# Kernel tuning notes

Hardware: AMD Instinct MI355X
Metric: run time of the kernel (lower is better)

## Reference

```python
import jax, jax.numpy as jnp
import numpy as np

N = 50000      # rows of A == cols of A (square constraint/variable graph)
NNZ = 1_600_000
D = 128        # x_size == y_size == out_size (forced by the module's wiring)


def spmm(rows, cols, vals, X, n_out):
    # out[r] = sum_{e: rows[e]==r} vals[e] * X[cols[e]]
    return jax.ops.segment_sum(vals[:, None] * X[cols], rows, num_segments=n_out)


def _linear(z, w, b):
    return z @ w.T + b


def setup_inputs() -> dict:
    key = jax.random.key(0)
    ks = jax.random.split(key, 20)
    f = lambda i, shape, s=1.0: jax.random.normal(ks[i], shape, dtype=jnp.float32) * s
    w_scale = 1.0 / np.sqrt(D)
    return {
        "x": f(0, (N, D)),
        "y": f(1, (N, D)),
        "c": f(2, (N, 1)),
        "b": f(3, (N, 1)),
        "A_vals": f(4, (NNZ,)),
        "A_rows": jax.random.randint(ks[5], (NNZ,), 0, N),
        "A_cols": jax.random.randint(ks[6], (NNZ,), 0, N),
        "Ukx_w": f(7, (D, D), w_scale), "Ukx_b": f(8, (D,), w_scale),
        "Uky_w": f(9, (D, D), w_scale), "Uky_b": f(10, (D,), w_scale),
        "tau": f(11, (1,)),
        "Vky_w": f(12, (D, D), w_scale), "Vky_b": f(13, (D,), w_scale),
        "Wkx_w": f(14, (D, D), w_scale), "Wkx_b": f(15, (D,), w_scale),
        "Vkx_w": f(16, (D, D), w_scale), "Vkx_b": f(17, (D,), w_scale),
        "sigma": f(18, (1,)),
    }


def reference(x, y, c, b, A_vals, A_rows, A_cols,
              Ukx_w, Ukx_b, Uky_w, Uky_b, tau,
              Vky_w, Vky_b, Wkx_w, Wkx_b, Vkx_w, Vkx_b, sigma):
    # --- pdhg_layer_x: x <- relu(Ukx(x) - tau * (c @ ones(1,D) - AT @ Uky(y))) ---
    # c @ ones(1, D) is just broadcasting c:[N,1] to [N,D].
    uy = _linear(y, Uky_w, Uky_b)                      # [N, D]
    at_uy = spmm(A_cols, A_rows, A_vals, uy, N)        # AT spmm: swap row/col indices
    x_new = jax.nn.relu(_linear(x, Ukx_w, Ukx_b) - tau * (c - at_uy))

    # --- pdhg_layer_y: y <- relu(Vky(y) - sigma * (b@ones - 2*A@Wkx(x') + A@Vkx(x'))) ---
    wx = _linear(x_new, Wkx_w, Wkx_b)                  # [N, D]
    vx = _linear(x_new, Vkx_w, Vkx_b)                  # [N, D]
    a_wx = spmm(A_rows, A_cols, A_vals, wx, N)
    a_vx = spmm(A_rows, A_cols, A_vals, vx, N)
    y_new = jax.nn.relu(_linear(y, Vky_w, Vky_b) - sigma * (b - 2.0 * a_wx + a_vx))
    return (x_new, y_new)
```

## Files before the change

### kernel.cpp

```cpp
#include <hip/hip_runtime.h>

#define D 128
#define RB 64
#define NBKMAX 1024
#define CH 256

__device__ __forceinline__ unsigned short bf16r(float f) {
    unsigned b = __float_as_uint(f);
    return (unsigned short)((b + 0x7FFFu + ((b >> 16) & 1u)) >> 16);
}

__global__ __launch_bounds__(256) void setup_weights(
    const float* __restrict__ Uky, const float* __restrict__ Ukx,
    const float* __restrict__ Vky, const float* __restrict__ Vkx,
    const float* __restrict__ Wkx, const float* __restrict__ Vkx_b,
    const float* __restrict__ Wkx_b,
    float* __restrict__ UkyT, float* __restrict__ UkxT,
    float* __restrict__ VkyT, float* __restrict__ WcT, float* __restrict__ bc)
{
    const int m = blockIdx.x;
    const float* src = (m == 0) ? Uky : (m == 1) ? Ukx : (m == 2) ? Vky : nullptr;
    float* dst = (m == 0) ? UkyT : (m == 1) ? UkxT : (m == 2) ? VkyT : WcT;
    for (int i = threadIdx.x; i < D * D; i += 256) {
        int k = i >> 7, d = i & 127;
        float v;
        if (m == 3) v = Vkx[d * D + k] - 2.0f * Wkx[d * D + k];
        else        v = src[d * D + k];
        dst[i] = v;
    }
    if (m == 3 && threadIdx.x < D)
        bc[threadIdx.x] = Vkx_b[threadIdx.x] - 2.0f * Wkx_b[threadIdx.x];
}

template <int EPI, int OB16>
__global__ __launch_bounds__(256) void gemm_v2(
    const float* __restrict__ X, const float* __restrict__ WT,
    const float* __restrict__ bias, const float* __restrict__ colvec,
    const float* __restrict__ spout, const float* __restrict__ scal,
    float* __restrict__ out, int N)
{
    __shared__ float Xs[64][D + 4];
    __shared__ float Wt[64][D + 4];
    const int t = threadIdx.x;
    const int block_row = blockIdx.x * 64;

#pragma unroll
    for (int i = 0; i < 8; ++i) {
        int f = t + i * 256;
        int r = f >> 5;
        int k4 = (f & 31) << 2;
        float4 g = make_float4(0.f, 0.f, 0.f, 0.f);
        int row = block_row + r;
        if (row < N) g = *reinterpret_cast<const float4*>(&X[(size_t)row * D + k4]);
        *reinterpret_cast<float4*>(&Xs[r][k4]) = g;
    }

    const int cg = t & 15;
    const int rp = t >> 4;
    const int r0 = rp * 4;
    const int c0 = cg * 4, c1 = 64 + cg * 4;

    float acc[4][8] = {{0.f}};

    for (int kb = 0; kb < D; kb += 64) {
        __syncthreads();
#pragma unroll
        for (int i = 0; i < 8; ++i) {
            int f = t + i * 256;
            int kk = f >> 5;
            int d4 = (f & 31) << 2;
            float4 g = *reinterpret_cast<const float4*>(&WT[(size_t)(kb + kk) * D + d4]);
            *reinterpret_cast<float4*>(&Wt[kk][d4]) = g;
        }
        __syncthreads();
#pragma unroll 2
        for (int k4 = 0; k4 < 64; k4 += 4) {
            float4 xr[4];
#pragma unroll
            for (int j = 0; j < 4; ++j)
                xr[j] = *reinterpret_cast<const float4*>(&Xs[r0 + j][kb + k4]);
#pragma unroll
            for (int q = 0; q < 4; ++q) {
                const float4 w0 = *reinterpret_cast<const float4*>(&Wt[k4 + q][c0]);
                const float4 w1 = *reinterpret_cast<const float4*>(&Wt[k4 + q][c1]);
#pragma unroll
                for (int j = 0; j < 4; ++j) {
                    const float xv = (q == 0) ? xr[j].x : (q == 1) ? xr[j].y
                                   : (q == 2) ? xr[j].z : xr[j].w;
                    acc[j][0] += xv * w0.x; acc[j][1] += xv * w0.y;
                    acc[j][2] += xv * w0.z; acc[j][3] += xv * w0.w;
                    acc[j][4] += xv * w1.x; acc[j][5] += xv * w1.y;
                    acc[j][6] += xv * w1.z; acc[j][7] += xv * w1.w;
                }
            }
        }
    }

    const float sc = (EPI == 0) ? 0.f : scal[0];
    const float4 bias0 = *reinterpret_cast<const float4*>(&bias[c0]);
    const float4 bias1 = *reinterpret_cast<const float4*>(&bias[c1]);

#pragma unroll
    for (int j = 0; j < 4; ++j) {
        const int row = block_row + r0 + j;
        if (row >= N) continue;
        const float cv = (EPI == 0) ? 0.f : colvec[row];
#pragma unroll
        for (int h = 0; h < 2; ++h) {
            const int col = (h == 0) ? c0 : c1;
            const float4 bs = (h == 0) ? bias0 : bias1;
            float4 res;
            res.x = acc[j][h * 4 + 0] + bs.x;
            res.y = acc[j][h * 4 + 1] + bs.y;
            res.z = acc[j][h * 4 + 2] + bs.z;
            res.w = acc[j][h * 4 + 3] + bs.w;
            if (EPI == 1) {
                float4 sp = *reinterpret_cast<const float4*>(&spout[(size_t)row * D + col]);
                res.x = fmaxf(res.x - sc * (cv - sp.x), 0.f);
                res.y = fmaxf(res.y - sc * (cv - sp.y), 0.f);
                res.z = fmaxf(res.z - sc * (cv - sp.z), 0.f);
                res.w = fmaxf(res.w - sc * (cv - sp.w), 0.f);
            } else if (EPI == 2) {
                float4 sp = *reinterpret_cast<const float4*>(&spout[(size_t)row * D + col]);
                res.x = fmaxf(res.x - sc * (cv + sp.x), 0.f);
                res.y = fmaxf(res.y - sc * (cv + sp.y), 0.f);
                res.z = fmaxf(res.z - sc * (cv + sp.z), 0.f);
                res.w = fmaxf(res.w - sc * (cv + sp.w), 0.f);
            }
            if (OB16) {
                unsigned short* ob = (unsigned short*)out;
                ushort4 r16;
                r16.x = bf16r(res.x); r16.y = bf16r(res.y);
                r16.z = bf16r(res.z); r16.w = bf16r(res.w);
                *reinterpret_cast<ushort4*>(&ob[(size_t)row * D + col]) = r16;
            } else {
                *reinterpret_cast<float4*>(&out[(size_t)row * D + col]) = res;
            }
        }
    }
}

__global__ __launch_bounds__(256) void hist_chunks(
    const int* __restrict__ rows, const int* __restrict__ cols,
    int* __restrict__ hR, int* __restrict__ hC, int nnz, int nbk, int ce)
{
    __shared__ int lh[NBKMAX];
    const int chunk = blockIdx.x;
    const bool isC = blockIdx.y;
    const int* idx = isC ? cols : rows;
    int* hout = (isC ? hC : hR) + (size_t)chunk * nbk;
    for (int i = threadIdx.x; i < nbk; i += 256) lh[i] = 0;
    __syncthreads();
    const int e0 = chunk * ce, e1 = min(nnz, e0 + ce);
    for (int e = e0 + threadIdx.x; e < e1; e += 256)
        atomicAdd(&lh[idx[e] >> 6], 1);
    __syncthreads();
    for (int i = threadIdx.x; i < nbk; i += 256) hout[i] = lh[i];
}

__global__ __launch_bounds__(256) void bucket_tot(
    const int* __restrict__ hR, const int* __restrict__ hC,
    int* __restrict__ cntR, int* __restrict__ cntC, int nbk)
{
    const int b = blockIdx.x;
    const bool isC = blockIdx.y;
    const int* h = (isC ? hC : hR);
    __shared__ int s[256];
    int v = h[(size_t)threadIdx.x * nbk + b];
    s[threadIdx.x] = v;
    __syncthreads();
#pragma unroll
    for (int d = 128; d > 0; d >>= 1) {
        if (threadIdx.x < d) s[threadIdx.x] += s[threadIdx.x + d];
        __syncthreads();
    }
    if (threadIdx.x == 0) (isC ? cntC : cntR)[b] = s[0];
}

__global__ __launch_bounds__(256) void scan_buckets(
    const int* __restrict__ cntR, const int* __restrict__ cntC,
    int* __restrict__ goffR, int* __restrict__ goffC, int nbk)
{
    const int* cnt = blockIdx.x ? cntC : cntR;
    int* goff = blockIdx.x ? goffC : goffR;
    __shared__ int s[256];
    const int t = threadIdx.x;
    const int base = t * 4;
    int loc[4]; int sum = 0;
#pragma unroll
    for (int u = 0; u < 4; ++u) {
        int idx = base + u;
        int v = (idx < nbk) ? cnt[idx] : 0;
        loc[u] = sum; sum += v;
    }
    s[t] = sum;
    __syncthreads();
#pragma unroll
    for (int d = 1; d < 256; d <<= 1) {
        int tv = (t >= d) ? s[t - d] : 0;
        __syncthreads();
        s[t] += tv;
        __syncthreads();
    }
    int excl = s[t] - sum;
#pragma unroll
    for (int u = 0; u < 4; ++u) {
        int idx = base + u;
        if (idx < nbk) goff[idx] = excl + loc[u];
    }
}

__global__ __launch_bounds__(256) void runstarts(
    int* __restrict__ hR, int* __restrict__ hC,
    const int* __restrict__ goffR, const int* __restrict__ goffC, int nbk)
{
    const int b = blockIdx.x;
    const bool isC = blockIdx.y;
    int* h = (isC ? hC : hR);
    const int g0 = (isC ? goffC : goffR)[b];
    __shared__ int s[256];
    const int t = threadIdx.x;
    int v = h[(size_t)t * nbk + b];
    s[t] = v;
    __syncthreads();
#pragma unroll
    for (int d = 1; d < 256; d <<= 1) {
        int tv = (t >= d) ? s[t - d] : 0;
        __syncthreads();
        s[t] += tv;
        __syncthreads();
    }
    h[(size_t)t * nbk + b] = g0 + s[t] - v;
}

__global__ __launch_bounds__(256) void scatter_chunks(
    const int* __restrict__ rows, const int* __restrict__ cols,
    const float* __restrict__ vals,
    const int* __restrict__ rsR, int2* __restrict__ recR,
    const int* __restrict__ rsC, int2* __restrict__ recC,
    int nnz, int nbk, int ce)
{
    __shared__ int lrsR[NBKMAX], lcurR[NBKMAX];
    __shared__ int lrsC[NBKMAX], lcurC[NBKMAX];
    const int chunk = blockIdx.x;
    for (int i = threadIdx.x; i < nbk; i += 256) {
        lrsR[i] = rsR[(size_t)chunk * nbk + i]; lcurR[i] = 0;
        lrsC[i] = rsC[(size_t)chunk * nbk + i]; lcurC[i] = 0;
    }
    __syncthreads();
    const int e0 = chunk * ce, e1 = min(nnz, e0 + ce);
    for (int e = e0 + threadIdx.x; e < e1; e += 256) {
        int r = rows[e], c = cols[e];
        int vb = __float_as_int(vals[e]);
        int bR = r >> 6, bC = c >> 6;
        int pR = lrsR[bR] + atomicAdd(&lcurR[bR], 1);
        recR[pR] = make_int2(((r & 63) << 16) | c, vb);
        int pC = lrsC[bC] + atomicAdd(&lcurC[bC], 1);
        recC[pC] = make_int2(((c & 63) << 16) | r, vb);
    }
}

__global__ __launch_bounds__(256) void sort_buckets(
    const int2* __restrict__ recR, const int2* __restrict__ recC,
    const int* __restrict__ goffR, const int* __restrict__ cntR,
    const int* __restrict__ goffC, const int* __restrict__ cntC,
    unsigned* __restrict__ pairsR, unsigned* __restrict__ pairsC,
    int* __restrict__ offR, int* __restrict__ lenR,
    int* __restrict__ offC, int* __restrict__ lenC, int N)
{
    const bool isC = blockIdx.y;
    const int b = blockIdx.x;
    const int2* rec = isC ? recC : recR;
    unsigned* pairs = isC ? pairsC : pairsR;
    int* off = isC ? offC : offR;
    int* len = isC ? lenC : lenR;
    const int s = (isC ? goffC : goffR)[b];
    const int L = (isC ? cntC : cntR)[b];
    const int t = threadIdx.x;

    __shared__ int lcnt[RB], lpos[RB], lcur[RB];
    if (t < RB) lcnt[t] = 0;
    __syncthreads();
    for (int i = t; i < L; i += 256)
        atomicAdd(&lcnt[rec[s + i].x >> 16], 1);
    __syncthreads();
    if (t == 0) {
        int run = 0;
#pragma unroll
        for (int r = 0; r < RB; ++r) { lpos[r] = run; run += lcnt[r]; }
    }
    __syncthreads();
    if (t < RB) {
        int row = b * RB + t;
        if (row < N) { off[row] = s + lpos[t]; len[row] = lcnt[t]; }
        lcur[t] = 0;
    }
    __syncthreads();
    for (int i = t; i < L; i += 256) {
        int2 pr = rec[s + i];
        int r = pr.x >> 16;
        int p = lpos[r] + atomicAdd(&lcur[r], 1);
        unsigned vb = (unsigned)pr.y;
        unsigned v16 = (vb + 0x7FFFu + ((vb >> 16) & 1u)) >> 16;
        pairs[s + p] = (v16 << 16) | (unsigned)(pr.x & 0xFFFF);
    }
}

__global__ __launch_bounds__(256) void spmm_pairs_v3(
    const unsigned* __restrict__ pairs, const int* __restrict__ off,
    const int* __restrict__ len, const unsigned short* __restrict__ Xb,
    float* __restrict__ out, int N)
{
    const int row = (blockIdx.x * 256 + threadIdx.x) >> 6;
    if (row >= N) return;
    const int lane = threadIdx.x & 63;
    const int half = lane >> 5;
    const int cq = (lane & 31) << 2;
    const int s = off[row];
    const int L = len[row];

    float4 a0 = make_float4(0.f, 0.f, 0.f, 0.f);
    float4 a1 = make_float4(0.f, 0.f, 0.f, 0.f);
    float4 a2 = make_float4(0.f, 0.f, 0.f, 0.f);
    float4 a3 = make_float4(0.f, 0.f, 0.f, 0.f);

#define BF(u) __uint_as_float((unsigned)(u) << 16)
    int i = 0;
    for (; i + 7 < L; i += 8) {
        unsigned p0 = pairs[s + i + 0 + half];
        unsigned p1 = pairs[s + i + 2 + half];
        unsigned p2 = pairs[s + i + 4 + half];
        unsigned p3 = pairs[s + i + 6 + half];
        ushort4 x0 = *reinterpret_cast<const ushort4*>(&Xb[(size_t)(p0 & 0xFFFFu) * D + cq]);
        ushort4 x1 = *reinterpret_cast<const ushort4*>(&Xb[(size_t)(p1 & 0xFFFFu) * D + cq]);
        ushort4 x2 = *reinterpret_cast<const ushort4*>(&Xb[(size_t)(p2 & 0xFFFFu) * D + cq]);
        ushort4 x3 = *reinterpret_cast<const ushort4*>(&Xb[(size_t)(p3 & 0xFFFFu) * D + cq]);
        float v0 = __uint_as_float(p0 & 0xFFFF0000u);
        float v1 = __uint_as_float(p1 & 0xFFFF0000u);
        float v2 = __uint_as_float(p2 & 0xFFFF0000u);
        float v3 = __uint_as_float(p3 & 0xFFFF0000u);
        a0.x += v0 * BF(x0.x); a0.y += v0 * BF(x0.y); a0.z += v0 * BF(x0.z); a0.w += v0 * BF(x0.w);
        a1.x += v1 * BF(x1.x); a1.y += v1 * BF(x1.y); a1.z += v1 * BF(x1.z); a1.w += v1 * BF(x1.w);
        a2.x += v2 * BF(x2.x); a2.y += v2 * BF(x2.y); a2.z += v2 * BF(x2.z); a2.w += v2 * BF(x2.w);
        a3.x += v3 * BF(x3.x); a3.y += v3 * BF(x3.y); a3.z += v3 * BF(x3.z); a3.w += v3 * BF(x3.w);
    }
    for (; i < L; i += 2) {
        int e = i + half;
        unsigned p = (e < L) ? pairs[s + e] : 0u;
        ushort4 xv = *reinterpret_cast<const ushort4*>(&Xb[(size_t)(p & 0xFFFFu) * D + cq]);
        float v = __uint_as_float(p & 0xFFFF0000u);
        a0.x += v * BF(xv.x); a0.y += v * BF(xv.y); a0.z += v * BF(xv.z); a0.w += v * BF(xv.w);
    }
#undef BF

    float4 A;
    A.x = (a0.x + a1.x) + (a2.x + a3.x);
    A.y = (a0.y + a1.y) + (a2.y + a3.y);
    A.z = (a0.z + a1.z) + (a2.z + a3.z);
    A.w = (a0.w + a1.w) + (a2.w + a3.w);
    A.x += __shfl_xor(A.x, 32);
    A.y += __shfl_xor(A.y, 32);
    A.z += __shfl_xor(A.z, 32);
    A.w += __shfl_xor(A.w, 32);
    if (half == 0)
        *reinterpret_cast<float4*>(&out[(size_t)row * D + cq]) = A;
}

__global__ __launch_bounds__(256) void spmm_atomic(
    const float* __restrict__ vals, const int* __restrict__ orow,
    const int* __restrict__ gcol, const float* __restrict__ Xm,
    float* __restrict__ outm, int nnz)
{
    const int gwave = (blockIdx.x * 256 + threadIdx.x) >> 6;
    const int lane = threadIdx.x & 63;
    const int e0 = gwave * 4;
#pragma unroll
    for (int i = 0; i < 4; ++i) {
        int e = e0 + i;
        if (e >= nnz) break;
        float v = vals[e];
        int r = orow[e];
        int c = gcol[e];
        float2 xv = *reinterpret_cast<const float2*>(&Xm[(size_t)c * D + lane * 2]);
        unsafeAtomicAdd(&outm[(size_t)r * D + lane * 2 + 0], v * xv.x);
        unsafeAtomicAdd(&outm[(size_t)r * D + lane * 2 + 1], v * xv.y);
    }
}

extern "C" void kernel_launch(void* const* d_in, const int* in_sizes, int n_in,
                              void* d_out, int out_size, void* d_ws, size_t ws_size,
                              hipStream_t stream) {
    const float* x      = (const float*)d_in[0];
    const float* y      = (const float*)d_in[1];
    const float* c      = (const float*)d_in[2];
    const float* b      = (const float*)d_in[3];
    const float* A_vals = (const float*)d_in[4];
    const int*   A_rows = (const int*)d_in[5];
    const int*   A_cols = (const int*)d_in[6];
    const float* Ukx_w  = (const float*)d_in[7];
    const float* Ukx_b  = (const float*)d_in[8];
    const float* Uky_w  = (const float*)d_in[9];
    const float* Uky_b  = (const float*)d_in[10];
    const float* tau    = (const float*)d_in[11];
    const float* Vky_w  = (const float*)d_in[12];
    const float* Vky_b  = (const float*)d_in[13];
    const float* Wkx_w  = (const float*)d_in[14];
    const float* Wkx_b  = (const float*)d_in[15];
    const float* Vkx_w  = (const float*)d_in[16];
    const float* Vkx_b  = (const float*)d_in[17];
    const float* sigma  = (const float*)d_in[18];

    const int N   = in_sizes[0] / D;
    const int nnz = in_sizes[4];
    const int nbk = (N + RB - 1) / RB;

    float* out_x = (float*)d_out;
    float* out_y = out_x + (size_t)N * D;

    const int gemm_grid = (N + 63) / 64;
    const int ggrid = (N + 3) / 4;

    const size_t pool = (size_t)nnz;
    char* base = (char*)d_ws;
    float* tmp = (float*)base;
    int2* recR = (int2*)base;
    int2* recC = recR + pool;
    size_t region0 = (size_t)N * D * 4;
    if (2 * pool * 8 > region0) region0 = 2 * pool * 8;
    char* pers = base + region0;
    float* UkyT = (float*)pers;
    float* UkxT = UkyT + D * D;
    float* VkyT = UkxT + D * D;
    float* WcT  = VkyT + D * D;
    float* bc   = WcT + D * D;
    unsigned* pairsR = (unsigned*)(bc + D);
    unsigned* pairsC = pairsR + pool;
    int* cntR  = (int*)(pairsC + pool);
    int* cntC  = cntR + nbk;
    int* goffR = cntC + nbk;
    int* goffC = goffR + nbk;
    int* offR  = goffC + nbk;
    int* lenR  = offR + N;
    int* offC  = lenR + N;
    int* lenC  = offC + N;
    int* hR = (int*)pairsR;
    int* hC = hR + (size_t)CH * nbk;

    unsigned short* uyb = (unsigned short*)out_y;
    unsigned short* zxb = (unsigned short*)tmp;

    size_t need = region0 + (4 * (size_t)D * D + D) * 4 + 2 * pool * 4
                + (4 * (size_t)nbk + 4 * (size_t)N) * 4;
    bool h_fits = (size_t)2 * CH * nbk * 4 <= pool * 4;

    setup_weights<<<4, 256, 0, stream>>>(Uky_w, Ukx_w, Vky_w, Vkx_w, Wkx_w,
                                         Vkx_b, Wkx_b, UkyT, UkxT, VkyT, WcT, bc);

    if (N < 65536 && nbk <= NBKMAX && ws_size >= need && h_fits) {
        const int ce = (nnz + CH - 1) / CH;

        {
            dim3 g1(CH, 2);
            hist_chunks<<<g1, 256, 0, stream>>>(A_rows, A_cols, hR, hC, nnz, nbk, ce);
            dim3 g2(nbk, 2);
            bucket_tot<<<g2, 256, 0, stream>>>(hR, hC, cntR, cntC, nbk);
            scan_buckets<<<2, 256, 0, stream>>>(cntR, cntC, goffR, goffC, nbk);
            runstarts<<<g2, 256, 0, stream>>>(hR, hC, goffR, goffC, nbk);
            scatter_chunks<<<CH, 256, 0, stream>>>(A_rows, A_cols, A_vals,
                                                   hR, recR, hC, recC, nnz, nbk, ce);
            sort_buckets<<<g2, 256, 0, stream>>>(recR, recC, goffR, cntR, goffC, cntC,
                                                 pairsR, pairsC, offR, lenR, offC, lenC, N);
        }

        gemm_v2<0, 1><<<gemm_grid, 256, 0, stream>>>(y, UkyT, Uky_b, nullptr, nullptr, nullptr,
                                                     (float*)uyb, N);
        spmm_pairs_v3<<<ggrid, 256, 0, stream>>>(pairsC, offC, lenC, uyb, out_x, N);
        gemm_v2<1, 0><<<gemm_grid, 256, 0, stream>>>(x, UkxT, Ukx_b, c, out_x, tau, out_x, N);
        gemm_v2<0, 1><<<gemm_grid, 256, 0, stream>>>(out_x, WcT, bc, nullptr, nullptr, nullptr,
                                                     (float*)zxb, N);
        spmm_pairs_v3<<<ggrid, 256, 0, stream>>>(pairsR, offR, lenR, zxb, out_y, N);
        gemm_v2<2, 0><<<gemm_grid, 256, 0, stream>>>(y, VkyT, Vky_b, b, out_y, sigma, out_y, N);
    } else {
        const int spmm_grid = (nnz + 15) / 16;
        gemm_v2<0, 0><<<gemm_grid, 256, 0, stream>>>(y, UkyT, Uky_b, nullptr, nullptr, nullptr, tmp, N);
        hipMemsetAsync(out_x, 0, (size_t)N * D * sizeof(float), stream);
        spmm_atomic<<<spmm_grid, 256, 0, stream>>>(A_vals, A_cols, A_rows, tmp, out_x, nnz);
        gemm_v2<1, 0><<<gemm_grid, 256, 0, stream>>>(x, UkxT, Ukx_b, c, out_x, tau, out_x, N);
        gemm_v2<0, 0><<<gemm_grid, 256, 0, stream>>>(out_x, WcT, bc, nullptr, nullptr, nullptr, tmp, N);
        hipMemsetAsync(out_y, 0, (size_t)N * D * sizeof(float), stream);
        spmm_atomic<<<spmm_grid, 256, 0, stream>>>(A_vals, A_rows, A_cols, tmp, out_y, nnz);
        gemm_v2<2, 0><<<gemm_grid, 256, 0, stream>>>(y, VkyT, Vky_b, b, out_y, sigma, out_y, N);
    }
}
```

Baseline: 330.0 us.

## Use bf16 MFMA for dense linear layers and widen scatter blocks

Replaces the fp32 SIMT GEMM in the fast path with a bf16 MFMA kernel (16x16x32). It converts the X tile to bf16 into XOR-swizzled shared memory and reads the pre-converted bf16 weights directly from global memory. Setup now also builds bf16 copies of the weights, and the fallback path keeps the fp32 GEMM. Separately, scatter_chunks moves to 1024-thread blocks. The aim is less FMA-bound GEMM time, at the cost of bf16 rounding of inputs and weights and more shared-memory atomic contention per block in scatter.

New measurement: 293.9 us. 11.0% less time.

```diff
diff --git a/kernel.cpp b/kernel.cpp
--- a/kernel.cpp
+++ b/kernel.cpp
@@ -4,6 +4,9 @@
 #define RB 64
 #define NBKMAX 1024
 #define CH 256
+
+typedef __attribute__((ext_vector_type(4))) float f32x4;
+typedef __attribute__((ext_vector_type(8))) short bf16x8;
 
 __device__ __forceinline__ unsigned short bf16r(float f) {
     unsigned b = __float_as_uint(f);
@@ -16,31 +19,45 @@
     const float* __restrict__ Wkx, const float* __restrict__ Vkx_b,
     const float* __restrict__ Wkx_b,
     float* __restrict__ UkyT, float* __restrict__ UkxT,
-    float* __restrict__ VkyT, float* __restrict__ WcT, float* __restrict__ bc)
+    float* __restrict__ VkyT, float* __restrict__ WcT,
+    unsigned short* __restrict__ UkyB, unsigned short* __restrict__ UkxB,
+    unsigned short* __restrict__ VkyB, unsigned short* __restrict__ WcB,
+    float* __restrict__ bc)
 {
     const int m = blockIdx.x;
-    const float* src = (m == 0) ? Uky : (m == 1) ? Ukx : (m == 2) ? Vky : nullptr;
-    float* dst = (m == 0) ? UkyT : (m == 1) ? UkxT : (m == 2) ? VkyT : WcT;
-    for (int i = threadIdx.x; i < D * D; i += 256) {
-        int k = i >> 7, d = i & 127;
-        float v;
-        if (m == 3) v = Vkx[d * D + k] - 2.0f * Wkx[d * D + k];
-        else        v = src[d * D + k];
-        dst[i] = v;
-    }
-    if (m == 3 && threadIdx.x < D)
-        bc[threadIdx.x] = Vkx_b[threadIdx.x] - 2.0f * Wkx_b[threadIdx.x];
+    if (m < 4) {
+        const float* src = (m == 0) ? Uky : (m == 1) ? Ukx : (m == 2) ? Vky : nullptr;
+        float* dst = (m == 0) ? UkyT : (m == 1) ? UkxT : (m == 2) ? VkyT : WcT;
+        for (int i = threadIdx.x; i < D * D; i += 256) {
+            int k = i >> 7, d = i & 127;
+            float v;
+            if (m == 3) v = Vkx[d * D + k] - 2.0f * Wkx[d * D + k];
+            else        v = src[d * D + k];
+            dst[i] = v;
+        }
+        if (m == 3 && threadIdx.x < D)
+            bc[threadIdx.x] = Vkx_b[threadIdx.x] - 2.0f * Wkx_b[threadIdx.x];
+    } else {
+        const int mm = m - 4;
+        const float* src = (mm == 0) ? Uky : (mm == 1) ? Ukx : (mm == 2) ? Vky : nullptr;
+        unsigned short* dst = (mm == 0) ? UkyB : (mm == 1) ? UkxB : (mm == 2) ? VkyB : WcB;
+        for (int i = threadIdx.x; i < D * D; i += 256) {
+            float v;
+            if (mm == 3) v = Vkx[i] - 2.0f * Wkx[i];
+            else         v = src[i];
+            dst[i] = bf16r(v);
+        }
+    }
 }
 
 template <int EPI, int OB16>
-__global__ __launch_bounds__(256) void gemm_v2(
-    const float* __restrict__ X, const float* __restrict__ WT,
+__global__ __launch_bounds__(256) void gemm_mfma(
+    const float* __restrict__ X, const unsigned short* __restrict__ Wb,
     const float* __restrict__ bias, const float* __restrict__ colvec,
     const float* __restrict__ spout, const float* __restrict__ scal,
     float* __restrict__ out, int N)
 {
-    __shared__ float Xs[64][D + 4];
-    __shared__ float Wt[64][D + 4];
+    __shared__ __align__(16) unsigned short Xs[64 * 128];
     const int t = threadIdx.x;
     const int block_row = blockIdx.x * 64;
 
@@ -52,14 +69,90 @@
         float4 g = make_float4(0.f, 0.f, 0.f, 0.f);
         int row = block_row + r;
         if (row < N) g = *reinterpret_cast<const float4*>(&X[(size_t)row * D + k4]);
-        *reinterpret_cast<float4*>(&Xs[r][k4]) = g;
+        ushort4 h;
+        h.x = bf16r(g.x); h.y = bf16r(g.y); h.z = bf16r(g.z); h.w = bf16r(g.w);
+        unsigned byte = (unsigned)(k4 * 2) ^ ((unsigned)(r & 7) << 4);
+        *reinterpret_cast<ushort4*>((char*)Xs + r * 256 + byte) = h;
+    }
+    __syncthreads();
+
+    const int w  = t >> 6;
+    const int l  = t & 63;
+    const int lr = l & 15;
+    const int lq = l >> 4;
+
+    f32x4 acc[8];
+#pragma unroll
+    for (int nt = 0; nt < 8; ++nt) acc[nt] = (f32x4)(0.f);
+
+    const int arow = w * 16 + lr;
+
+#pragma unroll
+    for (int kc = 0; kc < 4; ++kc) {
+        unsigned abyte = ((unsigned)(kc * 64 + lq * 16)) ^ ((unsigned)(arow & 7) << 4);
+        bf16x8 a = *reinterpret_cast<const bf16x8*>((const char*)Xs + arow * 256 + abyte);
+#pragma unroll
+        for (int nt = 0; nt < 8; ++nt) {
+            bf16x8 b = *reinterpret_cast<const bf16x8*>(
+                &Wb[(size_t)(nt * 16 + lr) * D + kc * 32 + lq * 8]);
+            acc[nt] = __builtin_amdgcn_mfma_f32_16x16x32_bf16(a, b, acc[nt], 0, 0, 0);
+        }
+    }
+
+    const float sc = (EPI == 0) ? 0.f : scal[0];
+    float bs[8];
+#pragma unroll
+    for (int nt = 0; nt < 8; ++nt) bs[nt] = bias[nt * 16 + lr];
+
+#pragma unroll
+    for (int r = 0; r < 4; ++r) {
+        const int row = block_row + w * 16 + lq * 4 + r;
+        if (row >= N) continue;
+        const float cv = (EPI == 0) ? 0.f : colvec[row];
+#pragma unroll
+        for (int nt = 0; nt < 8; ++nt) {
+            const int col = nt * 16 + lr;
+            float res = acc[nt][r] + bs[nt];
+            if (EPI == 1) {
+                float sp = spout[(size_t)row * D + col];
+                res = fmaxf(res - sc * (cv - sp), 0.f);
+            } else if (EPI == 2) {
+                float sp = spout[(size_t)row * D + col];
+                res = fmaxf(res - sc * (cv + sp), 0.f);
+            }
+            if (OB16) ((unsigned short*)out)[(size_t)row * D + col] = bf16r(res);
+            else      out[(size_t)row * D + col] = res;
+        }
+    }
+}
+
+template <int EPI>
+__global__ __launch_bounds__(256) void gemm_v2(
+    const float* __restrict__ X, const float* __restrict__ WT,
+    const float* __restrict__ bias, const float* __restrict__ colvec,
+    const float* __restrict__ spout, const float* __restrict__ scal,
+    float* __restrict__ out, int N)
+{
+    __shared__ float Xsf[64][D + 4];
+    __shared__ float Wt[64][D + 4];
+    const int t = threadIdx.x;
+    const int block_row = blockIdx.x * 64;
+
+#pragma unroll
+    for (int i = 0; i < 8; ++i) {
+        int f = t + i * 256;
+        int r = f >> 5;
+        int k4 = (f & 31) << 2;
+        float4 g = make_float4(0.f, 0.f, 0.f, 0.f);
+        int row = block_row + r;
+        if (row < N) g = *reinterpret_cast<const float4*>(&X[(size_t)row * D + k4]);
+        *reinterpret_cast<float4*>(&Xsf[r][k4]) = g;
     }
 
     const int cg = t & 15;
     const int rp = t >> 4;
     const int r0 = rp * 4;
     const int c0 = cg * 4, c1 = 64 + cg * 4;
-
     float acc[4][8] = {{0.f}};
 
     for (int kb = 0; kb < D; kb += 64) {
@@ -78,7 +171,7 @@
             float4 xr[4];
 #pragma unroll
             for (int j = 0; j < 4; ++j)
-                xr[j] = *reinterpret_cast<const float4*>(&Xs[r0 + j][kb + k4]);
+                xr[j] = *reinterpret_cast<const float4*>(&Xsf[r0 + j][kb + k4]);
 #pragma unroll
             for (int q = 0; q < 4; ++q) {
                 const float4 w0 = *reinterpret_cast<const float4*>(&Wt[k4 + q][c0]);
@@ -108,12 +201,12 @@
 #pragma unroll
         for (int h = 0; h < 2; ++h) {
             const int col = (h == 0) ? c0 : c1;
-            const float4 bs = (h == 0) ? bias0 : bias1;
+            const float4 bsv = (h == 0) ? bias0 : bias1;
             float4 res;
-            res.x = acc[j][h * 4 + 0] + bs.x;
-            res.y = acc[j][h * 4 + 1] + bs.y;
-            res.z = acc[j][h * 4 + 2] + bs.z;
-            res.w = acc[j][h * 4 + 3] + bs.w;
+            res.x = acc[j][h * 4 + 0] + bsv.x;
+            res.y = acc[j][h * 4 + 1] + bsv.y;
+            res.z = acc[j][h * 4 + 2] + bsv.z;
+            res.w = acc[j][h * 4 + 3] + bsv.w;
             if (EPI == 1) {
                 float4 sp = *reinterpret_cast<const float4*>(&spout[(size_t)row * D + col]);
                 res.x = fmaxf(res.x - sc * (cv - sp.x), 0.f);
@@ -127,15 +220,7 @@
                 res.z = fmaxf(res.z - sc * (cv + sp.z), 0.f);
                 res.w = fmaxf(res.w - sc * (cv + sp.w), 0.f);
             }
-            if (OB16) {
-                unsigned short* ob = (unsigned short*)out;
-                ushort4 r16;
-                r16.x = bf16r(res.x); r16.y = bf16r(res.y);
-                r16.z = bf16r(res.z); r16.w = bf16r(res.w);
-                *reinterpret_cast<ushort4*>(&ob[(size_t)row * D + col]) = r16;
-            } else {
-                *reinterpret_cast<float4*>(&out[(size_t)row * D + col]) = res;
-            }
+            *reinterpret_cast<float4*>(&out[(size_t)row * D + col]) = res;
         }
     }
 }
@@ -233,7 +318,7 @@
     h[(size_t)t * nbk + b] = g0 + s[t] - v;
 }
 
-__global__ __launch_bounds__(256) void scatter_chunks(
+__global__ __launch_bounds__(1024) void scatter_chunks(
     const int* __restrict__ rows, const int* __restrict__ cols,
     const float* __restrict__ vals,
     const int* __restrict__ rsR, int2* __restrict__ recR,
@@ -243,13 +328,13 @@
     __shared__ int lrsR[NBKMAX], lcurR[NBKMAX];
     __shared__ int lrsC[NBKMAX], lcurC[NBKMAX];
     const int chunk = blockIdx.x;
-    for (int i = threadIdx.x; i < nbk; i += 256) {
+    for (int i = threadIdx.x; i < nbk; i += 1024) {
         lrsR[i] = rsR[(size_t)chunk * nbk + i]; lcurR[i] = 0;
         lrsC[i] = rsC[(size_t)chunk * nbk + i]; lcurC[i] = 0;
     }
     __syncthreads();
     const int e0 = chunk * ce, e1 = min(nnz, e0 + ce);
-    for (int e = e0 + threadIdx.x; e < e1; e += 256) {
+    for (int e = e0 + threadIdx.x; e < e1; e += 1024) {
         int r = rows[e], c = cols[e];
         int vb = __float_as_int(vals[e]);
         int bR = r >> 6, bC = c >> 6;
@@ -432,7 +517,11 @@
     float* UkxT = UkyT + D * D;
     float* VkyT = UkxT + D * D;
     float* WcT  = VkyT + D * D;
-    float* bc   = WcT + D * D;
+    unsigned short* UkyB = (unsigned short*)(WcT + D * D);
+    unsigned short* UkxB = UkyB + D * D;
+    unsigned short* VkyB = UkxB + D * D;
+    unsigned short* WcB  = VkyB + D * D;
+    float* bc = (float*)(WcB + D * D);
     unsigned* pairsR = (unsigned*)(bc + D);
     unsigned* pairsC = pairsR + pool;
     int* cntR  = (int*)(pairsC + pool);
@@ -449,12 +538,13 @@
     unsigned short* uyb = (unsigned short*)out_y;
     unsigned short* zxb = (unsigned short*)tmp;
 
-    size_t need = region0 + (4 * (size_t)D * D + D) * 4 + 2 * pool * 4
-                + (4 * (size_t)nbk + 4 * (size_t)N) * 4;
+    size_t need = region0 + (4 * (size_t)D * D + D) * 4 + 4 * (size_t)D * D * 2
+                + 2 * pool * 4 + (4 * (size_t)nbk + 4 * (size_t)N) * 4;
     bool h_fits = (size_t)2 * CH * nbk * 4 <= pool * 4;
 
-    setup_weights<<<4, 256, 0, stream>>>(Uky_w, Ukx_w, Vky_w, Vkx_w, Wkx_w,
-                                         Vkx_b, Wkx_b, UkyT, UkxT, VkyT, WcT, bc);
+    setup_weights<<<8, 256, 0, stream>>>(Uky_w, Ukx_w, Vky_w, Vkx_w, Wkx_w,
+                                         Vkx_b, Wkx_b, UkyT, UkxT, VkyT, WcT,
+                                         UkyB, UkxB, VkyB, WcB, bc);
 
     if (N < 65536 && nbk <= NBKMAX && ws_size >= need && h_fits) {
         const int ce = (nnz + CH - 1) / CH;
@@ -466,29 +556,29 @@
             bucket_tot<<<g2, 256, 0, stream>>>(hR, hC, cntR, cntC, nbk);
             scan_buckets<<<2, 256, 0, stream>>>(cntR, cntC, goffR, goffC, nbk);
             runstarts<<<g2, 256, 0, stream>>>(hR, hC, goffR, goffC, nbk);
-            scatter_chunks<<<CH, 256, 0, stream>>>(A_rows, A_cols, A_vals,
-                                                   hR, recR, hC, recC, nnz, nbk, ce);
+            scatter_chunks<<<CH, 1024, 0, stream>>>(A_rows, A_cols, A_vals,
+                                                    hR, recR, hC, recC, nnz, nbk, ce);
             sort_buckets<<<g2, 256, 0, stream>>>(recR, recC, goffR, cntR, goffC, cntC,
                                                  pairsR, pairsC, offR, lenR, offC, lenC, N);
         }
 
-        gemm_v2<0, 1><<<gemm_grid, 256, 0, stream>>>(y, UkyT, Uky_b, nullptr, nullptr, nullptr,
-                                                     (float*)uyb, N);
+        gemm_mfma<0, 1><<<gemm_grid, 256, 0, stream>>>(y, UkyB, Uky_b, nullptr, nullptr, nullptr,
+                                                       (float*)uyb, N);
         spmm_pairs_v3<<<ggrid, 256, 0, stream>>>(pairsC, offC, lenC, uyb, out_x, N);
-        gemm_v2<1, 0><<<gemm_grid, 256, 0, stream>>>(x, UkxT, Ukx_b, c, out_x, tau, out_x, N);
-        gemm_v2<0, 1><<<gemm_grid, 256, 0, stream>>>(out_x, WcT, bc, nullptr, nullptr, nullptr,
-                                                     (float*)zxb, N);
+        gemm_mfma<1, 0><<<gemm_grid, 256, 0, stream>>>(x, UkxB, Ukx_b, c, out_x, tau, out_x, N);
+        gemm_mfma<0, 1><<<gemm_grid, 256, 0, stream>>>(out_x, WcB, bc, nullptr, nullptr, nullptr,
+                                                       (float*)zxb, N);
         spmm_pairs_v3<<<ggrid, 256, 0, stream>>>(pairsR, offR, lenR, zxb, out_y, N);
-        gemm_v2<2, 0><<<gemm_grid, 256, 0, stream>>>(y, VkyT, Vky_b, b, out_y, sigma, out_y, N);
+        gemm_mfma<2, 0><<<gemm_grid, 256, 0, stream>>>(y, VkyB, Vky_b, b, out_y, sigma, out_y, N);
     } else {
         const int spmm_grid = (nnz + 15) / 16;
-        gemm_v2<0, 0><<<gemm_grid, 256, 0, stream>>>(y, UkyT, Uky_b, nullptr, nullptr, nullptr, tmp, N);
+        gemm_v2<0><<<gemm_grid, 256, 0, stream>>>(y, UkyT, Uky_b, nullptr, nullptr, nullptr, tmp, N);
         hipMemsetAsync(out_x, 0, (size_t)N * D * sizeof(float), stream);
         spmm_atomic<<<spmm_grid, 256, 0, stream>>>(A_vals, A_cols, A_rows, tmp, out_x, nnz);
-        gemm_v2<1, 0><<<gemm_grid, 256, 0, stream>>>(x, UkxT, Ukx_b, c, out_x, tau, out_x, N);
-        gemm_v2<0, 0><<<gemm_grid, 256, 0, stream>>>(out_x, WcT, bc, nullptr, nullptr, nullptr, tmp, N);
+        gemm_v2<1><<<gemm_grid, 256, 0, stream>>>(x, UkxT, Ukx_b, c, out_x, tau, out_x, N);
+        gemm_v2<0><<<gemm_grid, 256, 0, stream>>>(out_x, WcT, bc, nullptr, nullptr, nullptr, tmp, N);
         hipMemsetAsync(out_y, 0, (size_t)N * D * sizeof(float), stream);
         spmm_atomic<<<spmm_grid, 256, 0, stream>>>(A_vals, A_rows, A_cols, tmp, out_y, nnz);
-        gemm_v2<2, 0><<<gemm_grid, 256, 0, stream>>>(y, VkyT, Vky_b, b, out_y, sigma, out_y, N);
-    }
-}
+        gemm_v2<2><<<gemm_grid, 256, 0, stream>>>(y, VkyT, Vky_b, b, out_y, sigma, out_y, N);
+    }
+}
```
